# Kernel tuning notes

Measured on AMD Instinct MI355X. Metric: run time of the kernel, lower is better.

## Reference

```python
import jax, jax.numpy as jnp
import numpy as np

T = 2_097_152  # number of daily timesteps
S_INIT = 0.0   # initial store fraction (s_init in module)


def setup_inputs() -> dict:
    key = jax.random.key(0)
    k1, _ = jax.random.split(key)
    # columns: P (precipitation), E (potential evapotranspiration), mm/day scale
    x = jax.random.uniform(k1, (T, 2), dtype=jnp.float32) * 10.0
    x1 = jnp.full((1,), 350.0, dtype=jnp.float32)  # production-store capacity (mm)
    return {"x": x, "x1": x1}


def reference(x, x1):
    x1s = x1[0]
    P = x[:, 0]
    E = x[:, 1]
    p_n = jnp.maximum(P - E, 0.0)  # net precipitation
    e_n = jnp.maximum(E - P, 0.0)  # net evapotranspiration

    def step(s_store, pe):
        pn_t, en_t = pe
        tp = jnp.tanh(pn_t / x1s)
        te = jnp.tanh(en_t / x1s)
        r = s_store / x1s
        p_s = x1s * (1.0 - r ** 2) * tp / (1.0 + r * tp)
        e_s = s_store * (2.0 - r) * te / (1.0 + (1.0 - r) * te)
        s_store = s_store + p_s - e_s
        perc = s_store * (1.0 - (1.0 + (4.0 / 9.0 * s_store / x1s) ** 4) ** (-0.25))
        s_store = s_store - perc
        return s_store, (p_s, perc)

    s0 = jnp.float32(S_INIT) * x1s
    _, (p_s, perc) = jax.lax.scan(step, s0, (p_n, e_n))

    # out: [T, 6] = [P, E, p_n, e_n, p_s, perc]
    out = jnp.concatenate(
        [x, p_n[:, None], e_n[:, None], p_s[:, None], perc[:, None]], axis=1
    )
    mu = out.mean(axis=0)
    sigma = out.std(axis=0, ddof=1)  # torch.std uses Bessel correction
    return (out - mu) / sigma
```

## Files before the change

### kernel.cpp

```cpp
#include <hip/hip_runtime.h>


#define T_TOTAL   (1 << 21)
#define L_CHUNK   16
#define C_CHUNKS  (T_TOTAL / L_CHUNK)
#define NCOARSE   32
#define NTAIL     128
#define WPAD      40
#define THREADS   256
#define NBLOCKS   (C_CHUNKS / THREADS)
#define LDSN      4256
#define NSTAGE    2120
#define X4MAX     (T_TOTAL / 2 - 1)
#define C49       0.44444445f

#define OFF_PP    0
#define OFF_SP    32768
#define OFF_MUSIG 49152
#define OFF_S4    49664
#define OFF_SIDE  (OFF_S4 + (WPAD + C_CHUNKS) * 16)

#define SWZ(w) ((w) ^ (((w) >> 4) & 31))

__global__ __launch_bounds__(256, 2) void prepass_kernel(const float4* __restrict__ x4,
                                                         const float* __restrict__ x1p,
                                                         float4* __restrict__ s4,
                                                         double* __restrict__ pp) {
    const float x1s    = x1p[0];
    const float inv_x1 = 1.0f / x1s;
    const int w = blockIdx.x * 256 + threadIdx.x;
    const float4* px = x4 + 8 * (size_t)w;

    float Tp = 0, Qp = 0, Te = 0, Qe = 0;
    float s0 = 0, s1 = 0, s2c = 0, s3 = 0, q0 = 0, q1 = 0, q2 = 0, q3 = 0;
#pragma unroll
    for (int q = 0; q < 8; ++q) {
        float4 v = px[q];
        float pn0 = fmaxf(v.x - v.y, 0.0f), en0 = fmaxf(v.y - v.x, 0.0f);
        float pn1 = fmaxf(v.z - v.w, 0.0f), en1 = fmaxf(v.w - v.z, 0.0f);
        float a0 = pn0 * inv_x1, b0 = en0 * inv_x1;
        float a1 = pn1 * inv_x1, b1 = en1 * inv_x1;
        float tp0 = a0 * fmaf(a0 * a0, -0.33333334f, 1.0f);
        float te0 = b0 * fmaf(b0 * b0, -0.33333334f, 1.0f);
        float tp1 = a1 * fmaf(a1 * a1, -0.33333334f, 1.0f);
        float te1 = b1 * fmaf(b1 * b1, -0.33333334f, 1.0f);
        Tp += tp0 + tp1;  Te += te0 + te1;
        Qp = fmaf(tp0, tp0, Qp); Qp = fmaf(tp1, tp1, Qp);
        Qe = fmaf(te0, te0, Qe); Qe = fmaf(te1, te1, Qe);
        s0 += v.x + v.z; q0 = fmaf(v.x, v.x, q0); q0 = fmaf(v.z, v.z, q0);
        s1 += v.y + v.w; q1 = fmaf(v.y, v.y, q1); q1 = fmaf(v.w, v.w, q1);
        s2c += pn0 + pn1; q2 = fmaf(pn0, pn0, q2); q2 = fmaf(pn1, pn1, q2);
        s3 += en0 + en1; q3 = fmaf(en0, en0, q3); q3 = fmaf(en1, en1, q3);
    }
    float cc0 = Tp;
    float cc1 = 2.0f * (Qe - Te) - Qp;
    float cc2 = Te - Tp - 3.0f * Qe;
    float cc3 = Qp + Qe;
    s4[WPAD + w] = make_float4(cc0, cc1, cc2, cc3);
    if (blockIdx.x == 0 && threadIdx.x < WPAD)
        s4[threadIdx.x] = make_float4(0, 0, 0, 0);

    __shared__ double red[4][8];
    double vv[8] = {s0, s1, s2c, s3, q0, q1, q2, q3};
    const int wid = threadIdx.x >> 6, lane = threadIdx.x & 63;
#pragma unroll
    for (int c = 0; c < 8; ++c) {
        double val = vv[c];
        for (int off = 32; off > 0; off >>= 1) val += __shfl_down(val, off, 64);
        if (lane == 0) red[wid][c] = val;
    }
    __syncthreads();
    if (threadIdx.x < 8) {
        int c = threadIdx.x;
        pp[c * 512 + blockIdx.x] = red[0][c] + red[1][c] + red[2][c] + red[3][c];
    }
}

#define CL(v) fminf(fmaxf((v), 0.0f), rmax)

#define DRIFT(RV, C, OUT)                                                  \
    {                                                                      \
        float rr_ = (RV);                                                  \
        float d_ = fmaf(rr_, fmaf(rr_, fmaf(rr_, (C).w, (C).z), (C).y), (C).x); \
        float y_  = rr_ * C49;                                             \
        float y2_ = y_ * y_;                                               \
        float u_  = y2_ * y2_;                                             \
        float pl_ = fmaf(u_, fmaf(u_, 1.875f, -2.5f), 4.0f);               \
        OUT = d_ - (rr_ * u_) * pl_;                                       \
    }

#define CSTEP(C)                                                           \
    {                                                                      \
        float k1_, k2_;                                                    \
        DRIFT(r, C, k1_)                                                   \
        float sm_ = CL(r + k1_);                                           \
        DRIFT(sm_, C, k2_)                                                 \
        r = CL(fmaf(0.5f, k1_ + k2_, r));                                  \
    }

#define CGRP_R(OFF)                                                        \
    CSTEP(c0) c0 = ps4[(OFF) + 8];  CSTEP(c1) c1 = ps4[(OFF) + 9];         \
    CSTEP(c2) c2 = ps4[(OFF) + 10]; CSTEP(c3) c3 = ps4[(OFF) + 11];        \
    CSTEP(c4) c4 = ps4[(OFF) + 12]; CSTEP(c5) c5 = ps4[(OFF) + 13];        \
    CSTEP(c6) c6 = ps4[(OFF) + 14]; CSTEP(c7) c7 = ps4[(OFF) + 15];
#define CGRP_L                                                             \
    CSTEP(c0) CSTEP(c1) CSTEP(c2) CSTEP(c3)                                \
    CSTEP(c4) CSTEP(c5) CSTEP(c6) CSTEP(c7)

#define FSTEP(a, b2)                                                       \
    {                                                                      \
        float m_  = fmaf(-0.5f, (b2), (a));                       \
        float rn_ = r + fmaf(r, fmaf(r, -m_, -(b2)), (a));                 \
        float y_  = rn_ * C49; float y2_ = y_ * y_; float u_ = y2_ * y2_;  \
        float pl_ = fmaf(u_, -0.15625f, 0.25f);                            \
        r = rn_ - (rn_ * u_) * pl_;                                        \
    }

#define ESTEP(a, b2, PS, PC)                                               \
    {                                                                      \
        float b_   = 0.5f * (b2);                                          \
        float tp_  = (a) * fmaf((a) * (a), -0.33333334f, 1.0f);            \
        float te_  = b_ * fmaf(b_ * b_, -0.33333334f, 1.0f);               \
        float q1_  = fmaf(-r, tp_, 1.0f);                        \
        float dp_  = (tp_ * fmaf(-r, r, 1.0f)) * q1_;                      \
        float omr_ = 1.0f - r;                                             \
        float q2_  = fmaf(-te_, omr_, 1.0f);                     \
        float de_  = ((r * (2.0f - r)) * te_) * q2_;                       \
        float rn_  = r + (dp_ - de_);                                      \
        float y_   = rn_ * C49; float y2_ = y_ * y_; float u_ = y2_ * y2_; \
        float pl_  = fmaf(u_, fmaf(u_, 0.1171875f, -0.15625f), 0.25f);     \
        float pcr_ = (rn_ * u_) * pl_;                                     \
        r = rn_ - pcr_;                                                    \
        PS = x1s * dp_;                                                    \
        PC = x1s * pcr_;                                                   \
    }

#define RD(Sb, mm) (*(const float2*)(lbase + ((Sb) ^ ((mm) << 3))))

#define FQ(RN, mm)                                                         \
    FSTEP(RN.x, RN.y)                                                      \
    RN = ((mm) < 12) ? RD(Sc, (mm) + 4) : RD(Sn, (mm) - 12);

#define EPAIR2(RA, RB, m0)                                                 \
    {                                                                      \
        float psA, pcA, psB, pcB;                                          \
        ESTEP(RA.x, RA.y, psA, pcA)                                        \
        ESTEP(RB.x, RB.y, psB, pcB)                                        \
        if (SIDE) {                                                        \
            *(float4*)(side + 2 * (size_t)(t0 + (m0))) =                   \
                make_float4(psA, pcA, psB, pcB);                           \
        } else {                                                           \
            *(float2*)(out + 6 * (size_t)(t0 + (m0)) + 4)  = make_float2(psA, pcA); \
            *(float2*)(out + 6 * (size_t)(t0 + (m0)) + 10) = make_float2(psB, pcB); \
        }                                                                  \
        sum4 += psA + psB; sq4 = fmaf(psA, psA, sq4); sq4 = fmaf(psB, psB, sq4); \
        sum5 += pcA + pcB; sq5 = fmaf(pcA, pcA, sq5); sq5 = fmaf(pcB, pcB, sq5); \
        if ((m0) < 12) { RA = RD(Se, (m0) + 4); RB = RD(Se, (m0) + 5); }   \
    }

template <bool SIDE>
__global__ __launch_bounds__(256, 2) void scan_kernel(const float4* __restrict__ x4,
                                                      const float* __restrict__ x1p,
                                                      const float4* __restrict__ s4,
                                                      float* __restrict__ out,
                                                      float* __restrict__ side,
                                                      double* __restrict__ sp) {
    __shared__ float2 plane[LDSN];
    __shared__ double red[4][4];

    const float x1s    = x1p[0];
    const float inv_x1 = 1.0f / x1s;
    const float inv2x  = 2.0f * inv_x1;
    const float rmax   = 320.0f * inv_x1;
    const int k  = blockIdx.x * 256 + threadIdx.x;
    const int kp = threadIdx.x;
    const char* lbase = (const char*)plane;

    {
        const int g0 = 8 * (blockIdx.x * 256) - NTAIL / 2;
        for (int t = threadIdx.x; t < NSTAGE; t += 256) {
            int g4 = g0 + t;
            float4 v = x4[min(max(g4, 0), X4MAX)];
            float a0 = fmaxf(v.x - v.y, 0.0f) * inv_x1;
            float b0 = fmaxf(v.y - v.x, 0.0f) * inv2x;
            float a1 = fmaxf(v.z - v.w, 0.0f) * inv_x1;
            float b1 = fmaxf(v.w - v.z, 0.0f) * inv2x;
            if (g4 < 0) { a0 = b0 = a1 = b1 = 0.0f; }
            plane[SWZ(2 * t)]     = make_float2(a0, b0);
            plane[SWZ(2 * t + 1)] = make_float2(a1, b1);
        }
    }

    const float4* ps4 = s4 + k;
    float4 c0 = ps4[0], c1 = ps4[1], c2 = ps4[2], c3 = ps4[3],
           c4 = ps4[4], c5 = ps4[5], c6 = ps4[6], c7 = ps4[7];
    float r = 0.0f;
    CGRP_R(0) CGRP_R(8) CGRP_R(16) CGRP_L

    __syncthreads();

    float2 r0, r1, r2, r3;
    {
        const int S0 = SWZ(16 * kp) << 3;
        r0 = RD(S0, 0); r1 = RD(S0, 1); r2 = RD(S0, 2); r3 = RD(S0, 3);
    }
#pragma unroll 1
    for (int B = 0; B < NTAIL; B += 16) {
        const int W0 = 16 * kp + B;
        const int Sc = SWZ(W0) << 3;
        const int Sn = SWZ(W0 + 16) << 3;
        FQ(r0, 0)  FQ(r1, 1)  FQ(r2, 2)  FQ(r3, 3)
        FQ(r0, 4)  FQ(r1, 5)  FQ(r2, 6)  FQ(r3, 7)
        FQ(r0, 8)  FQ(r1, 9)  FQ(r2, 10) FQ(r3, 11)
        FQ(r0, 12) FQ(r1, 13) FQ(r2, 14) FQ(r3, 15)
    }

    float sum4 = 0, sum5 = 0, sq4 = 0, sq5 = 0;
    const int t0 = 16 * k;
    const int Se = SWZ(16 * kp + NTAIL) << 3;
    EPAIR2(r0, r1, 0)  EPAIR2(r2, r3, 2)
    EPAIR2(r0, r1, 4)  EPAIR2(r2, r3, 6)
    EPAIR2(r0, r1, 8)  EPAIR2(r2, r3, 10)
    EPAIR2(r0, r1, 12) EPAIR2(r2, r3, 14)

    double vv[4] = {sum4, sum5, sq4, sq5};
    const int wid = threadIdx.x >> 6, lane = threadIdx.x & 63;
#pragma unroll
    for (int c = 0; c < 4; ++c) {
        double val = vv[c];
        for (int off = 32; off > 0; off >>= 1) val += __shfl_down(val, off, 64);
        if (lane == 0) red[wid][c] = val;
    }
    __syncthreads();
    if (threadIdx.x < 4) {
        int c = threadIdx.x;
        sp[c * 512 + blockIdx.x] = red[0][c] + red[1][c] + red[2][c] + red[3][c];
    }
}

__global__ __launch_bounds__(256) void finalize_kernel(const double* __restrict__ pp,
                                                       const double* __restrict__ sp,
                                                       float* __restrict__ musig) {
    __shared__ double red[12][4];
    const int t = threadIdx.x, lane = t & 63, wid = t >> 6;
#pragma unroll
    for (int c = 0; c < 8; ++c) {
        double v = pp[c * 512 + t] + pp[c * 512 + 256 + t];
        for (int off = 32; off > 0; off >>= 1) v += __shfl_down(v, off, 64);
        if (lane == 0) red[c][wid] = v;
    }
#pragma unroll
    for (int c = 0; c < 4; ++c) {
        double v = sp[c * 512 + t] + sp[c * 512 + 256 + t];
        for (int off = 32; off > 0; off >>= 1) v += __shfl_down(v, off, 64);
        if (lane == 0) red[8 + c][wid] = v;
    }
    __syncthreads();
    if (t < 6) {
        int si = (t < 4) ? t : (4 + t);
        int qi = (t < 4) ? (4 + t) : (6 + t);
        double sum = red[si][0] + red[si][1] + red[si][2] + red[si][3];
        double sq  = red[qi][0] + red[qi][1] + red[qi][2] + red[qi][3];
        double n = (double)T_TOTAL;
        double mu = sum / n;
        double var = (sq - sum * sum / n) / (n - 1.0);
        musig[t] = (float)mu;
        musig[6 + t] = (float)(1.0 / sqrt(var));
    }
}

template <bool SIDE>
__global__ __launch_bounds__(256) void normalize_kernel(const float4* __restrict__ xp4,
                                                        const float4* __restrict__ side4,
                                                        float* __restrict__ out,
                                                        const float* __restrict__ musig) {
    float mu[6], is[6];
#pragma unroll
    for (int c = 0; c < 6; ++c) { mu[c] = musig[c]; is[c] = musig[6 + c]; }

    int idx = blockIdx.x * blockDim.x + threadIdx.x;
    int stride = gridDim.x * blockDim.x;
    for (int p = idx; p < T_TOTAL / 2; p += stride) {
        float4 xv = xp4[p];
        float* o = out + 12 * (size_t)p;
        float4 sv;
        if (SIDE) {
            sv = side4[p];
        } else {
            float2 a = *(const float2*)(o + 4);
            float2 b = *(const float2*)(o + 10);
            sv = make_float4(a.x, a.y, b.x, b.y);
        }
        float pn0 = fmaxf(xv.x - xv.y, 0.0f), en0 = fmaxf(xv.y - xv.x, 0.0f);
        float pn1 = fmaxf(xv.z - xv.w, 0.0f), en1 = fmaxf(xv.w - xv.z, 0.0f);
        float4 o0 = {(xv.x - mu[0]) * is[0], (xv.y - mu[1]) * is[1],
                     (pn0 - mu[2]) * is[2], (en0 - mu[3]) * is[3]};
        float4 o1 = {(sv.x - mu[4]) * is[4], (sv.y - mu[5]) * is[5],
                     (xv.z - mu[0]) * is[0], (xv.w - mu[1]) * is[1]};
        float4 o2 = {(pn1 - mu[2]) * is[2], (en1 - mu[3]) * is[3],
                     (sv.z - mu[4]) * is[4], (sv.w - mu[5]) * is[5]};
        *(float4*)(o + 0) = o0;
        *(float4*)(o + 4) = o1;
        *(float4*)(o + 8) = o2;
    }
}

extern "C" void kernel_launch(void* const* d_in, const int* in_sizes, int n_in,
                              void* d_out, int out_size, void* d_ws, size_t ws_size,
                              hipStream_t stream) {
    const float4* x4 = (const float4*)d_in[0];
    const float* x1 = (const float*)d_in[1];
    float* out = (float*)d_out;
    char* ws = (char*)d_ws;
    double* pp = (double*)(ws + OFF_PP);
    double* sp = (double*)(ws + OFF_SP);
    float* musig = (float*)(ws + OFF_MUSIG);
    float4* s4 = (float4*)(ws + OFF_S4);
    float* side = (float*)(ws + OFF_SIDE);

    const bool use_side = ws_size >= (size_t)OFF_SIDE + (size_t)T_TOTAL * 8;

    prepass_kernel<<<NBLOCKS, THREADS, 0, stream>>>(x4, x1, s4, pp);
    if (use_side) {
        scan_kernel<true><<<NBLOCKS, THREADS, 0, stream>>>(x4, x1, s4, out, side, sp);
        finalize_kernel<<<1, 256, 0, stream>>>(pp, sp, musig);
        normalize_kernel<true><<<2048, 256, 0, stream>>>(x4, (const float4*)side, out, musig);
    } else {
        scan_kernel<false><<<NBLOCKS, THREADS, 0, stream>>>(x4, x1, s4, out, side, sp);
        finalize_kernel<<<1, 256, 0, stream>>>(pp, sp, musig);
        normalize_kernel<false><<<2048, 256, 0, stream>>>(x4, (const float4*)side, out, musig);
    }
}
```

Measured before the change: 52.86 us.

## Fuse prepass into scan kernel, computing chunk coefficients from LDS window

```diff
diff --git a/kernel.cpp b/kernel.cpp
--- a/kernel.cpp
+++ b/kernel.cpp
@@ -2,79 +2,23 @@
 
 
 #define T_TOTAL   (1 << 21)
-#define L_CHUNK   16
-#define C_CHUNKS  (T_TOTAL / L_CHUNK)
+#define C_CHUNKS  (T_TOTAL / 16)
 #define NCOARSE   32
 #define NTAIL     128
-#define WPAD      40
 #define THREADS   256
 #define NBLOCKS   (C_CHUNKS / THREADS)
-#define LDSN      4256
-#define NSTAGE    2120
+#define NSTAGE4   2376
+#define LDSN      4768
+#define NWIN      287
 #define X4MAX     (T_TOTAL / 2 - 1)
 #define C49       0.44444445f
 
-#define OFF_PP    0
-#define OFF_SP    32768
+#define OFF_SP    0
 #define OFF_MUSIG 49152
-#define OFF_S4    49664
-#define OFF_SIDE  (OFF_S4 + (WPAD + C_CHUNKS) * 16)
+#define OFF_SIDE  49664
 
 #define SWZ(w) ((w) ^ (((w) >> 4) & 31))
-
-__global__ __launch_bounds__(256, 2) void prepass_kernel(const float4* __restrict__ x4,
-                                                         const float* __restrict__ x1p,
-                                                         float4* __restrict__ s4,
-                                                         double* __restrict__ pp) {
-    const float x1s    = x1p[0];
-    const float inv_x1 = 1.0f / x1s;
-    const int w = blockIdx.x * 256 + threadIdx.x;
-    const float4* px = x4 + 8 * (size_t)w;
-
-    float Tp = 0, Qp = 0, Te = 0, Qe = 0;
-    float s0 = 0, s1 = 0, s2c = 0, s3 = 0, q0 = 0, q1 = 0, q2 = 0, q3 = 0;
-#pragma unroll
-    for (int q = 0; q < 8; ++q) {
-        float4 v = px[q];
-        float pn0 = fmaxf(v.x - v.y, 0.0f), en0 = fmaxf(v.y - v.x, 0.0f);
-        float pn1 = fmaxf(v.z - v.w, 0.0f), en1 = fmaxf(v.w - v.z, 0.0f);
-        float a0 = pn0 * inv_x1, b0 = en0 * inv_x1;
-        float a1 = pn1 * inv_x1, b1 = en1 * inv_x1;
-        float tp0 = a0 * fmaf(a0 * a0, -0.33333334f, 1.0f);
-        float te0 = b0 * fmaf(b0 * b0, -0.33333334f, 1.0f);
-        float tp1 = a1 * fmaf(a1 * a1, -0.33333334f, 1.0f);
-        float te1 = b1 * fmaf(b1 * b1, -0.33333334f, 1.0f);
-        Tp += tp0 + tp1;  Te += te0 + te1;
-        Qp = fmaf(tp0, tp0, Qp); Qp = fmaf(tp1, tp1, Qp);
-        Qe = fmaf(te0, te0, Qe); Qe = fmaf(te1, te1, Qe);
-        s0 += v.x + v.z; q0 = fmaf(v.x, v.x, q0); q0 = fmaf(v.z, v.z, q0);
-        s1 += v.y + v.w; q1 = fmaf(v.y, v.y, q1); q1 = fmaf(v.w, v.w, q1);
-        s2c += pn0 + pn1; q2 = fmaf(pn0, pn0, q2); q2 = fmaf(pn1, pn1, q2);
-        s3 += en0 + en1; q3 = fmaf(en0, en0, q3); q3 = fmaf(en1, en1, q3);
-    }
-    float cc0 = Tp;
-    float cc1 = 2.0f * (Qe - Te) - Qp;
-    float cc2 = Te - Tp - 3.0f * Qe;
-    float cc3 = Qp + Qe;
-    s4[WPAD + w] = make_float4(cc0, cc1, cc2, cc3);
-    if (blockIdx.x == 0 && threadIdx.x < WPAD)
-        s4[threadIdx.x] = make_float4(0, 0, 0, 0);
-
-    __shared__ double red[4][8];
-    double vv[8] = {s0, s1, s2c, s3, q0, q1, q2, q3};
-    const int wid = threadIdx.x >> 6, lane = threadIdx.x & 63;
-#pragma unroll
-    for (int c = 0; c < 8; ++c) {
-        double val = vv[c];
-        for (int off = 32; off > 0; off >>= 1) val += __shfl_down(val, off, 64);
-        if (lane == 0) red[wid][c] = val;
-    }
-    __syncthreads();
-    if (threadIdx.x < 8) {
-        int c = threadIdx.x;
-        pp[c * 512 + blockIdx.x] = red[0][c] + red[1][c] + red[2][c] + red[3][c];
-    }
-}
+#define RD(Sb, mm) (*(const float2*)(lbase + ((Sb) ^ ((mm) << 3))))
 
 #define CL(v) fminf(fmaxf((v), 0.0f), rmax)
 
@@ -98,11 +42,13 @@
         r = CL(fmaf(0.5f, k1_ + k2_, r));                                  \
     }
 
+#define WLD(j) make_float4(cA[kp + (j)], cB[kp + (j)], cC[kp + (j)], cD[kp + (j)])
+
 #define CGRP_R(OFF)                                                        \
-    CSTEP(c0) c0 = ps4[(OFF) + 8];  CSTEP(c1) c1 = ps4[(OFF) + 9];         \
-    CSTEP(c2) c2 = ps4[(OFF) + 10]; CSTEP(c3) c3 = ps4[(OFF) + 11];        \
-    CSTEP(c4) c4 = ps4[(OFF) + 12]; CSTEP(c5) c5 = ps4[(OFF) + 13];        \
-    CSTEP(c6) c6 = ps4[(OFF) + 14]; CSTEP(c7) c7 = ps4[(OFF) + 15];
+    CSTEP(c0) c0 = WLD((OFF) + 8);  CSTEP(c1) c1 = WLD((OFF) + 9);         \
+    CSTEP(c2) c2 = WLD((OFF) + 10); CSTEP(c3) c3 = WLD((OFF) + 11);        \
+    CSTEP(c4) c4 = WLD((OFF) + 12); CSTEP(c5) c5 = WLD((OFF) + 13);        \
+    CSTEP(c6) c6 = WLD((OFF) + 14); CSTEP(c7) c7 = WLD((OFF) + 15);
 #define CGRP_L                                                             \
     CSTEP(c0) CSTEP(c1) CSTEP(c2) CSTEP(c3)                                \
     CSTEP(c4) CSTEP(c5) CSTEP(c6) CSTEP(c7)
@@ -135,8 +81,6 @@
         PC = x1s * pcr_;                                                   \
     }
 
-#define RD(Sb, mm) (*(const float2*)(lbase + ((Sb) ^ ((mm) << 3))))
-
 #define FQ(RN, mm)                                                         \
     FSTEP(RN.x, RN.y)                                                      \
     RN = ((mm) < 12) ? RD(Sc, (mm) + 4) : RD(Sn, (mm) - 12);
@@ -161,12 +105,12 @@
 template <bool SIDE>
 __global__ __launch_bounds__(256, 2) void scan_kernel(const float4* __restrict__ x4,
                                                       const float* __restrict__ x1p,
-                                                      const float4* __restrict__ s4,
                                                       float* __restrict__ out,
                                                       float* __restrict__ side,
                                                       double* __restrict__ sp) {
     __shared__ float2 plane[LDSN];
-    __shared__ double red[4][4];
+    __shared__ float cA[NWIN + 1], cB[NWIN + 1], cC[NWIN + 1], cD[NWIN + 1];
+    __shared__ double red[4][12];
 
     const float x1s    = x1p[0];
     const float inv_x1 = 1.0f / x1s;
@@ -176,37 +120,60 @@
     const int kp = threadIdx.x;
     const char* lbase = (const char*)plane;
 
+    float s0 = 0, s1 = 0, s2c = 0, s3 = 0, q0 = 0, q1 = 0, q2 = 0, q3 = 0;
     {
-        const int g0 = 8 * (blockIdx.x * 256) - NTAIL / 2;
-        for (int t = threadIdx.x; t < NSTAGE; t += 256) {
-            int g4 = g0 + t;
-            float4 v = x4[min(max(g4, 0), X4MAX)];
-            float a0 = fmaxf(v.x - v.y, 0.0f) * inv_x1;
-            float b0 = fmaxf(v.y - v.x, 0.0f) * inv2x;
-            float a1 = fmaxf(v.z - v.w, 0.0f) * inv_x1;
-            float b1 = fmaxf(v.w - v.z, 0.0f) * inv2x;
-            if (g4 < 0) { a0 = b0 = a1 = b1 = 0.0f; }
-            plane[SWZ(2 * t)]     = make_float2(a0, b0);
-            plane[SWZ(2 * t + 1)] = make_float2(a1, b1);
+        const int g0 = 2048 * blockIdx.x - 320;
+        for (int j = 0; j < 10; ++j) {
+            int ts = threadIdx.x + 256 * j;
+            if (ts < NSTAGE4) {
+                int g4 = g0 + ts;
+                float4 v = x4[min(max(g4, 0), X4MAX)];
+                float pn0 = fmaxf(v.x - v.y, 0.0f), en0 = fmaxf(v.y - v.x, 0.0f);
+                float pn1 = fmaxf(v.z - v.w, 0.0f), en1 = fmaxf(v.w - v.z, 0.0f);
+                if (g4 < 0) { pn0 = en0 = pn1 = en1 = 0.0f; }
+                plane[SWZ(2 * ts)]     = make_float2(pn0 * inv_x1, en0 * inv2x);
+                plane[SWZ(2 * ts + 1)] = make_float2(pn1 * inv_x1, en1 * inv2x);
+                if (ts >= 320 && ts < 2368) {
+                    s0 += v.x + v.z; q0 = fmaf(v.x, v.x, q0); q0 = fmaf(v.z, v.z, q0);
+                    s1 += v.y + v.w; q1 = fmaf(v.y, v.y, q1); q1 = fmaf(v.w, v.w, q1);
+                    s2c += pn0 + pn1; q2 = fmaf(pn0, pn0, q2); q2 = fmaf(pn1, pn1, q2);
+                    s3 += en0 + en1; q3 = fmaf(en0, en0, q3); q3 = fmaf(en1, en1, q3);
+                }
+            }
         }
     }
-
-    const float4* ps4 = s4 + k;
-    float4 c0 = ps4[0], c1 = ps4[1], c2 = ps4[2], c3 = ps4[3],
-           c4 = ps4[4], c5 = ps4[5], c6 = ps4[6], c7 = ps4[7];
+    __syncthreads();
+
+    for (int wl = threadIdx.x; wl < NWIN; wl += 256) {
+        const int Sw = SWZ(16 * wl) << 3;
+        float Sa = 0, Sa2 = 0, Sb = 0, Sb2 = 0;
+#pragma unroll
+        for (int mm = 0; mm < 16; ++mm) {
+            float2 p = RD(Sw, mm);
+            Sa += p.x; Sa2 = fmaf(p.x, p.x, Sa2);
+            Sb += p.y; Sb2 = fmaf(p.y, p.y, Sb2);
+        }
+        float Tp = Sa, Qp = Sa2, Te = 0.5f * Sb, Qe = 0.25f * Sb2;
+        cA[wl] = Tp;
+        cB[wl] = 2.0f * (Qe - Te) - Qp;
+        cC[wl] = Te - Tp - 3.0f * Qe;
+        cD[wl] = Qp + Qe;
+    }
+    __syncthreads();
+
+    float4 c0 = WLD(0), c1 = WLD(1), c2 = WLD(2), c3 = WLD(3),
+           c4 = WLD(4), c5 = WLD(5), c6 = WLD(6), c7 = WLD(7);
     float r = 0.0f;
     CGRP_R(0) CGRP_R(8) CGRP_R(16) CGRP_L
 
-    __syncthreads();
-
     float2 r0, r1, r2, r3;
     {
-        const int S0 = SWZ(16 * kp) << 3;
+        const int S0 = SWZ(16 * kp + 512) << 3;
         r0 = RD(S0, 0); r1 = RD(S0, 1); r2 = RD(S0, 2); r3 = RD(S0, 3);
     }
 #pragma unroll 1
     for (int B = 0; B < NTAIL; B += 16) {
-        const int W0 = 16 * kp + B;
+        const int W0 = 16 * kp + 512 + B;
         const int Sc = SWZ(W0) << 3;
         const int Sn = SWZ(W0 + 16) << 3;
         FQ(r0, 0)  FQ(r1, 1)  FQ(r2, 2)  FQ(r3, 3)
@@ -217,50 +184,42 @@
 
     float sum4 = 0, sum5 = 0, sq4 = 0, sq5 = 0;
     const int t0 = 16 * k;
-    const int Se = SWZ(16 * kp + NTAIL) << 3;
+    const int Se = SWZ(16 * kp + 512 + NTAIL) << 3;
     EPAIR2(r0, r1, 0)  EPAIR2(r2, r3, 2)
     EPAIR2(r0, r1, 4)  EPAIR2(r2, r3, 6)
     EPAIR2(r0, r1, 8)  EPAIR2(r2, r3, 10)
     EPAIR2(r0, r1, 12) EPAIR2(r2, r3, 14)
 
-    double vv[4] = {sum4, sum5, sq4, sq5};
+    double vv[12] = {s0, s1, s2c, s3, sum4, sum5,
+                     q0, q1, q2, q3, sq4, sq5};
     const int wid = threadIdx.x >> 6, lane = threadIdx.x & 63;
 #pragma unroll
-    for (int c = 0; c < 4; ++c) {
+    for (int c = 0; c < 12; ++c) {
         double val = vv[c];
         for (int off = 32; off > 0; off >>= 1) val += __shfl_down(val, off, 64);
         if (lane == 0) red[wid][c] = val;
     }
     __syncthreads();
-    if (threadIdx.x < 4) {
+    if (threadIdx.x < 12) {
         int c = threadIdx.x;
         sp[c * 512 + blockIdx.x] = red[0][c] + red[1][c] + red[2][c] + red[3][c];
     }
 }
 
-__global__ __launch_bounds__(256) void finalize_kernel(const double* __restrict__ pp,
-                                                       const double* __restrict__ sp,
+__global__ __launch_bounds__(256) void finalize_kernel(const double* __restrict__ sp,
                                                        float* __restrict__ musig) {
     __shared__ double red[12][4];
     const int t = threadIdx.x, lane = t & 63, wid = t >> 6;
 #pragma unroll
-    for (int c = 0; c < 8; ++c) {
-        double v = pp[c * 512 + t] + pp[c * 512 + 256 + t];
+    for (int c = 0; c < 12; ++c) {
+        double v = sp[c * 512 + t] + sp[c * 512 + 256 + t];
         for (int off = 32; off > 0; off >>= 1) v += __shfl_down(v, off, 64);
         if (lane == 0) red[c][wid] = v;
     }
-#pragma unroll
-    for (int c = 0; c < 4; ++c) {
-        double v = sp[c * 512 + t] + sp[c * 512 + 256 + t];
-        for (int off = 32; off > 0; off >>= 1) v += __shfl_down(v, off, 64);
-        if (lane == 0) red[8 + c][wid] = v;
-    }
     __syncthreads();
     if (t < 6) {
-        int si = (t < 4) ? t : (4 + t);
-        int qi = (t < 4) ? (4 + t) : (6 + t);
-        double sum = red[si][0] + red[si][1] + red[si][2] + red[si][3];
-        double sq  = red[qi][0] + red[qi][1] + red[qi][2] + red[qi][3];
+        double sum = red[t][0] + red[t][1] + red[t][2] + red[t][3];
+        double sq  = red[6 + t][0] + red[6 + t][1] + red[6 + t][2] + red[6 + t][3];
         double n = (double)T_TOTAL;
         double mu = sum / n;
         double var = (sq - sum * sum / n) / (n - 1.0);
@@ -312,22 +271,19 @@
     const float* x1 = (const float*)d_in[1];
     float* out = (float*)d_out;
     char* ws = (char*)d_ws;
-    double* pp = (double*)(ws + OFF_PP);
     double* sp = (double*)(ws + OFF_SP);
     float* musig = (float*)(ws + OFF_MUSIG);
-    float4* s4 = (float4*)(ws + OFF_S4);
     float* side = (float*)(ws + OFF_SIDE);
 
     const bool use_side = ws_size >= (size_t)OFF_SIDE + (size_t)T_TOTAL * 8;
 
-    prepass_kernel<<<NBLOCKS, THREADS, 0, stream>>>(x4, x1, s4, pp);
     if (use_side) {
-        scan_kernel<true><<<NBLOCKS, THREADS, 0, stream>>>(x4, x1, s4, out, side, sp);
-        finalize_kernel<<<1, 256, 0, stream>>>(pp, sp, musig);
+        scan_kernel<true><<<NBLOCKS, THREADS, 0, stream>>>(x4, x1, out, side, sp);
+        finalize_kernel<<<1, 256, 0, stream>>>(sp, musig);
         normalize_kernel<true><<<2048, 256, 0, stream>>>(x4, (const float4*)side, out, musig);
     } else {
-        scan_kernel<false><<<NBLOCKS, THREADS, 0, stream>>>(x4, x1, s4, out, side, sp);
-        finalize_kernel<<<1, 256, 0, stream>>>(pp, sp, musig);
+        scan_kernel<false><<<NBLOCKS, THREADS, 0, stream>>>(x4, x1, out, side, sp);
+        finalize_kernel<<<1, 256, 0, stream>>>(sp, musig);
         normalize_kernel<false><<<2048, 256, 0, stream>>>(x4, (const float4*)side, out, musig);
     }
 }
```

Result: faster. 48.96 us (-7.4%).
